# Performance work log

Measured on AMD Instinct MI355X. Metric: run time of the kernel, lower is better.

## Reference

```python
import jax, jax.numpy as jnp
import numpy as np

B, S, D, H = 4, 2048, 512, 8
DK = D // H  # 64


def setup_inputs() -> dict:
    key = jax.random.key(0)
    ks = jax.random.split(key, 7)
    return {
        "q": jax.random.normal(ks[0], (B, S, D), dtype=jnp.float32),
        "k": jax.random.normal(ks[1], (B, S, D), dtype=jnp.float32),
        "v": jax.random.normal(ks[2], (B, S, D), dtype=jnp.float32),
        # per-head query projection weights (also used for k and v, replicating
        # the source's bug where q_linear projects all three inputs)
        "Wq": jax.random.normal(ks[3], (H, DK, D), dtype=jnp.float32) * (1.0 / np.sqrt(D)),
        "bq": jax.random.normal(ks[4], (H, DK), dtype=jnp.float32) * 0.02,
        "Wout": jax.random.normal(ks[5], (D, H * DK), dtype=jnp.float32) * (1.0 / np.sqrt(D)),
        "bout": jax.random.normal(ks[6], (D,), dtype=jnp.float32) * 0.02,
    }


def reference(q, k, v, Wq, bq, Wout, bout):
    # Per-head projections, batched over heads. NOTE: the original module
    # (buggy but faithful) applies the SAME q_linear to q, k and v.
    scale = 1.0 / jnp.sqrt(jnp.asarray(Wq.shape[1], dtype=q.dtype))
    qh = jnp.einsum("bsd,hed->bhse", q, Wq) + bq[:, None, :]  # [B,H,S,DK]
    kh = jnp.einsum("bsd,hed->bhse", k, Wq) + bq[:, None, :]
    vh = jnp.einsum("bsd,hed->bhse", v, Wq) + bq[:, None, :]
    scores = jnp.einsum("bhqe,bhke->bhqk", qh, kh) * scale  # [B,H,S,S]
    weights = jax.nn.softmax(scores, axis=-1)
    heads = jnp.einsum("bhqk,bhke->bhqe", weights, vh)  # [B,H,S,DK]
    # concat heads along feature dim (head-major order matches torch.cat)
    concat = heads.transpose(0, 2, 1, 3).reshape(q.shape[0], q.shape[1], -1)
    return concat @ Wout.T + bout
```

## Files before the change

kernel.cpp:

```cpp
#include <hip/hip_runtime.h>

#define BB 4
#define SS 2048
#define DD 512
#define HH 8
#define DKK 64
#define HDK 512

typedef __attribute__((ext_vector_type(4))) float f32x4;
typedef __attribute__((ext_vector_type(8))) __bf16 bf16x8;
typedef __attribute__((ext_vector_type(4))) __bf16 bf16x4;

#define MFMA16(a, b, c) __builtin_amdgcn_mfma_f32_16x16x32_bf16((a), (b), (c), 0, 0, 0)

#define GLOAD_LDS16(gptr, lptr)                                                    \
    __builtin_amdgcn_global_load_lds(                                              \
        (const __attribute__((address_space(1))) void*)(gptr),                     \
        (__attribute__((address_space(3))) void*)(lptr), 16, 0, 0)

__device__ inline bf16x8 cvt48(const f32x4 f0, const f32x4 f1) {
    bf16x8 w;
    w[0] = (__bf16)f0[0]; w[1] = (__bf16)f0[1]; w[2] = (__bf16)f0[2]; w[3] = (__bf16)f0[3];
    w[4] = (__bf16)f1[0]; w[5] = (__bf16)f1[1]; w[6] = (__bf16)f1[2]; w[7] = (__bf16)f1[3];
    return w;
}

__global__ __launch_bounds__(256) void proj_kernel(
    const float* __restrict__ q, const float* __restrict__ k, const float* __restrict__ v,
    const float* __restrict__ Wq, const float* __restrict__ bq,
    __bf16* __restrict__ qh, __bf16* __restrict__ kh, __bf16* __restrict__ vt)
{
    const int z  = blockIdx.z;
    const float* X = (z == 0) ? q : (z == 1) ? k : v;
    const int m0 = blockIdx.x * 128;
    const int n0 = blockIdx.y * 128;

    __shared__ __align__(16) float As[128 * 64];
    __shared__ __align__(16) float Bs[128 * 64];

    const int t    = threadIdx.x;
    const int lane = t & 63, wid = t >> 6;
    const int lo   = lane & 15, hi = lane >> 4;
    const int wm   = wid >> 1, wn = wid & 1;

    const int srofs  = lane >> 4;
    const int schunk = lane & 15;

    f32x4 acc[4][4] = {};

    for (int k0 = 0; k0 < DD; k0 += 64) {
        __syncthreads();
#pragma unroll
        for (int i = 0; i < 8; ++i) {
            const int r0  = 32 * wid + 4 * i;
            const int row = r0 + srofs;
            const int gco = ((schunk ^ (row & 7)) << 4);
            GLOAD_LDS16((const char*)&X [(size_t)(m0 + row) * DD + k0] + gco,
                        (char*)As + r0 * 256);
            GLOAD_LDS16((const char*)&Wq[(size_t)(n0 + row) * DD + k0] + gco,
                        (char*)Bs + r0 * 256);
        }
        __syncthreads();

#pragma unroll
        for (int kk = 0; kk < 2; ++kk) {
            bf16x8 a[4], b[4];
#pragma unroll
            for (int mi = 0; mi < 4; ++mi) {
                const int ar = wm * 64 + mi * 16 + lo;
                const int rs = (ar & 7) << 4;
                const int cb = kk * 128 + hi * 32;
                f32x4 f0 = *reinterpret_cast<const f32x4*>((const char*)As + ar * 256 + (cb ^ rs));
                f32x4 f1 = *reinterpret_cast<const f32x4*>((const char*)As + ar * 256 + ((cb + 16) ^ rs));
                a[mi] = cvt48(f0, f1);
            }
#pragma unroll
            for (int ni = 0; ni < 4; ++ni) {
                const int br = wn * 64 + ni * 16 + lo;
                const int rs = (br & 7) << 4;
                const int cb = kk * 128 + hi * 32;
                f32x4 f0 = *reinterpret_cast<const f32x4*>((const char*)Bs + br * 256 + (cb ^ rs));
                f32x4 f1 = *reinterpret_cast<const f32x4*>((const char*)Bs + br * 256 + ((cb + 16) ^ rs));
                b[ni] = cvt48(f0, f1);
            }
#pragma unroll
            for (int mi = 0; mi < 4; ++mi)
#pragma unroll
                for (int ni = 0; ni < 4; ++ni)
                    acc[mi][ni] = MFMA16(a[mi], b[ni], acc[mi][ni]);
        }
    }

#pragma unroll
    for (int mi = 0; mi < 4; ++mi) {
#pragma unroll
        for (int ni = 0; ni < 4; ++ni) {
            const int n = n0 + wn * 64 + ni * 16 + lo;
            const float bias = bq[n];
            const int h_ = n >> 6, e_ = n & 63;
#pragma unroll
            for (int r = 0; r < 4; ++r) {
                const int m = m0 + wm * 64 + mi * 16 + hi * 4 + r;
                const float val = acc[mi][ni][r] + bias;
                const int b_ = m >> 11, s_ = m & (SS - 1);
                const size_t bh = (size_t)(b_ * HH + h_);
                if (z == 0)
                    qh[(bh * SS + s_) * DKK + e_] = (__bf16)val;
                else if (z == 1)
                    kh[(bh * SS + s_) * DKK + e_] = (__bf16)val;
                else
                    vt[(bh * DKK + e_) * SS + s_] = (__bf16)val;
            }
        }
    }
}

__global__ __launch_bounds__(256) void attn_kernel(
    const __bf16* __restrict__ qh, const __bf16* __restrict__ kh,
    const __bf16* __restrict__ vt, __bf16* __restrict__ concat)
{
    const int q0 = blockIdx.x * 64;
    const int bh = blockIdx.y;
    const int b_ = bh >> 3, h_ = bh & 7;
    const size_t base = (size_t)bh * SS * DKK;
    const __bf16* qhp = qh + base;
    const __bf16* khp = kh + base;
    const __bf16* vtp = vt + base;

    const int t    = threadIdx.x;
    const int lane = t & 63, wid = t >> 6;
    const int lo   = lane & 15, hi = lane >> 4;

    __shared__ __align__(16) __bf16 Ks[64 * 64];
    __shared__ __align__(16) __bf16 Vts[64 * 64];
    __shared__ __align__(16) __bf16 Ps[4][16][72];

    char* KsB  = (char*)Ks;
    char* VtsB = (char*)Vts;

    const int sr   = lane >> 3;
    const int gcb  = (lane & 7) << 4;
    const int scb  = gcb ^ (sr << 4);
    const int srow = 16 * wid + sr;

    bf16x8 qf[2];
#pragma unroll
    for (int kk = 0; kk < 2; ++kk)
        qf[kk] = *reinterpret_cast<const bf16x8*>(
            &qhp[(size_t)(q0 + 16 * wid + lo) * DKK + 32 * kk + 8 * hi]);

    f32x4 acc[4] = {};
    float m_run = -INFINITY, l_run = 0.f;

    for (int kv0 = 0; kv0 < SS; kv0 += 64) {
        bf16x8 kr0 = *reinterpret_cast<const bf16x8*>(
            (const char*)&khp[(size_t)(kv0 + srow) * DKK] + gcb);
        bf16x8 kr1 = *reinterpret_cast<const bf16x8*>(
            (const char*)&khp[(size_t)(kv0 + srow + 8) * DKK] + gcb);
        bf16x8 vr0 = *reinterpret_cast<const bf16x8*>(
            (const char*)&vtp[(size_t)srow * SS + kv0] + gcb);
        bf16x8 vr1 = *reinterpret_cast<const bf16x8*>(
            (const char*)&vtp[(size_t)(srow + 8) * SS + kv0] + gcb);

        __syncthreads();
        *reinterpret_cast<bf16x8*>(KsB  + srow * 128 + scb)       = kr0;
        *reinterpret_cast<bf16x8*>(KsB  + (srow + 8) * 128 + scb) = kr1;
        *reinterpret_cast<bf16x8*>(VtsB + srow * 128 + scb)       = vr0;
        *reinterpret_cast<bf16x8*>(VtsB + (srow + 8) * 128 + scb) = vr1;
        __syncthreads();

        f32x4 sc[4] = {};
#pragma unroll
        for (int kk = 0; kk < 2; ++kk) {
            bf16x8 kf[4];
#pragma unroll
            for (int f = 0; f < 4; ++f) {
                const int row = 16 * f + lo;
                const int cb  = (64 * kk + 16 * hi) ^ ((row & 7) << 4);
                kf[f] = *reinterpret_cast<const bf16x8*>(KsB + row * 128 + cb);
            }
#pragma unroll
            for (int f = 0; f < 4; ++f)
                sc[f] = MFMA16(kf[f], qf[kk], sc[f]);
        }

        {
            float mx = -1e30f;
#pragma unroll
            for (int f = 0; f < 4; ++f)
#pragma unroll
                for (int r = 0; r < 4; ++r)
                    mx = fmaxf(mx, sc[f][r]);
            mx = fmaxf(mx, __shfl_xor(mx, 16));
            mx = fmaxf(mx, __shfl_xor(mx, 32));
            const float mnew = fmaxf(m_run, mx * 0.125f);
            const float scl  = __expf(m_run - mnew);
            float rs = 0.f;
#pragma unroll
            for (int f = 0; f < 4; ++f) {
                bf16x4 pk;
#pragma unroll
                for (int r = 0; r < 4; ++r) {
                    const float e = __expf(fmaf(sc[f][r], 0.125f, -mnew));
                    rs += e;
                    pk[r] = (__bf16)e;
                }
                *reinterpret_cast<bf16x4*>(&Ps[wid][lo][16 * f + 4 * hi]) = pk;
            }
            rs += __shfl_xor(rs, 16);
            rs += __shfl_xor(rs, 32);
            l_run = l_run * scl + rs;
            m_run = mnew;
#pragma unroll
            for (int f = 0; f < 4; ++f)
                acc[f] *= scl;
        }

#pragma unroll
        for (int kk = 0; kk < 2; ++kk) {
            bf16x8 pb = *reinterpret_cast<const bf16x8*>(&Ps[wid][lo][32 * kk + 8 * hi]);
#pragma unroll
            for (int f = 0; f < 4; ++f) {
                const int row = 16 * f + lo;
                const int cb  = (64 * kk + 16 * hi) ^ ((row & 7) << 4);
                bf16x8 vf = *reinterpret_cast<const bf16x8*>(VtsB + row * 128 + cb);
                acc[f] = MFMA16(vf, pb, acc[f]);
            }
        }
    }

    {
        const float inv = 1.0f / l_run;
        const int qrow = q0 + 16 * wid + lo;
        const size_t ob = ((size_t)b_ * SS + qrow) * HDK + h_ * DKK;
#pragma unroll
        for (int f = 0; f < 4; ++f) {
            bf16x4 o;
#pragma unroll
            for (int r = 0; r < 4; ++r)
                o[r] = (__bf16)(acc[f][r] * inv);
            *reinterpret_cast<bf16x4*>(&concat[ob + 16 * f + 4 * hi]) = o;
        }
    }
}

__global__ __launch_bounds__(256) void outproj_kernel(
    const __bf16* __restrict__ concat, const float* __restrict__ Wout,
    const float* __restrict__ bout, float* __restrict__ out)
{
    const int m0 = blockIdx.x * 128;
    const int n0 = blockIdx.y * 128;

    __shared__ __align__(16) __bf16 As[128 * 64];
    __shared__ __align__(16) float  Bs[128 * 64];

    const int t    = threadIdx.x;
    const int lane = t & 63, wid = t >> 6;
    const int lo   = lane & 15, hi = lane >> 4;
    const int wm   = wid >> 1, wn = wid & 1;

    f32x4 acc[4][4] = {};

    for (int k0 = 0; k0 < HDK; k0 += 64) {
        __syncthreads();
#pragma unroll
        for (int i = 0; i < 4; ++i) {
            const int r0  = 32 * wid + 8 * i;
            const int row = r0 + (lane >> 3);
            const int gco = ((lane & 7) ^ (row & 7)) << 4;
            GLOAD_LDS16((const char*)&concat[(size_t)(m0 + row) * HDK + k0] + gco,
                        (char*)As + r0 * 128);
        }
#pragma unroll
        for (int i = 0; i < 8; ++i) {
            const int r0  = 32 * wid + 4 * i;
            const int row = r0 + (lane >> 4);
            const int gco = ((lane & 15) ^ (row & 7)) << 4;
            GLOAD_LDS16((const char*)&Wout[(size_t)(n0 + row) * HDK + k0] + gco,
                        (char*)Bs + r0 * 256);
        }
        __syncthreads();

#pragma unroll
        for (int kk = 0; kk < 2; ++kk) {
            bf16x8 a[4], b[4];
#pragma unroll
            for (int mi = 0; mi < 4; ++mi) {
                const int ar = wm * 64 + mi * 16 + lo;
                const int cb = (kk * 64 + hi * 16) ^ ((ar & 7) << 4);
                a[mi] = *reinterpret_cast<const bf16x8*>((const char*)As + ar * 128 + cb);
            }
#pragma unroll
            for (int ni = 0; ni < 4; ++ni) {
                const int br = wn * 64 + ni * 16 + lo;
                const int rs = (br & 7) << 4;
                const int cb = kk * 128 + hi * 32;
                f32x4 f0 = *reinterpret_cast<const f32x4*>((const char*)Bs + br * 256 + (cb ^ rs));
                f32x4 f1 = *reinterpret_cast<const f32x4*>((const char*)Bs + br * 256 + ((cb + 16) ^ rs));
                b[ni] = cvt48(f0, f1);
            }
#pragma unroll
            for (int mi = 0; mi < 4; ++mi)
#pragma unroll
                for (int ni = 0; ni < 4; ++ni)
                    acc[mi][ni] = MFMA16(a[mi], b[ni], acc[mi][ni]);
        }
    }

#pragma unroll
    for (int mi = 0; mi < 4; ++mi) {
#pragma unroll
        for (int ni = 0; ni < 4; ++ni) {
            const int n = n0 + wn * 64 + ni * 16 + lo;
            const float bias = bout[n];
#pragma unroll
            for (int r = 0; r < 4; ++r) {
                const int m = m0 + wm * 64 + mi * 16 + hi * 4 + r;
                out[(size_t)m * DD + n] = acc[mi][ni][r] + bias;
            }
        }
    }
}

extern "C" void kernel_launch(void* const* d_in, const int* in_sizes, int n_in,
                              void* d_out, int out_size, void* d_ws, size_t ws_size,
                              hipStream_t stream)
{
    (void)in_sizes; (void)n_in; (void)out_size; (void)ws_size;
    const float* q    = (const float*)d_in[0];
    const float* k    = (const float*)d_in[1];
    const float* v    = (const float*)d_in[2];
    const float* Wq   = (const float*)d_in[3];
    const float* bq   = (const float*)d_in[4];
    const float* Wout = (const float*)d_in[5];
    const float* bout = (const float*)d_in[6];
    float* out = (float*)d_out;

    char* ws = (char*)d_ws;
    __bf16* qh = (__bf16*)(ws);
    __bf16* kh = (__bf16*)(ws + (8u << 20));
    __bf16* vt = (__bf16*)(ws + (16u << 20));
    __bf16* cc = (__bf16*)(ws + (24u << 20));

    proj_kernel<<<dim3(BB * SS / 128, HDK / 128, 3), 256, 0, stream>>>(q, k, v, Wq, bq, qh, kh, vt);
    attn_kernel<<<dim3(SS / 64, BB * HH), 256, 0, stream>>>(qh, kh, vt, cc);
    outproj_kernel<<<dim3(BB * SS / 128, DD / 128), 256, 0, stream>>>(cc, Wout, bout, out);
}
```

Before: 223.8 us.

## Double-buffer projection GEMMs, widen attention KV tile, add lazy softmax rescale

The projection and output-projection GEMMs switch to double-buffered LDS with 32-wide k-steps. Each next tile's async global-to-LDS load is issued before computing the current tile, so there is one barrier per step instead of two. The output projection halves its M tile to 64 rows, which doubles its grid. Attention processes 128 keys per iteration, skips the running-max rescale unless the max grows by more than a threshold, and raises wave priority around MFMA blocks. These changes cut synchronisation and exposed load latency, at the cost of more LDS and a possible small accuracy loss from the lazy rescale.

```diff
diff --git a/kernel.cpp b/kernel.cpp
--- a/kernel.cpp
+++ b/kernel.cpp
@@ -35,60 +35,67 @@
     const int m0 = blockIdx.x * 128;
     const int n0 = blockIdx.y * 128;
 
-    __shared__ __align__(16) float As[128 * 64];
-    __shared__ __align__(16) float Bs[128 * 64];
+    __shared__ __align__(16) float As0[128 * 32], Bs0[128 * 32];
+    __shared__ __align__(16) float As1[128 * 32], Bs1[128 * 32];
 
     const int t    = threadIdx.x;
     const int lane = t & 63, wid = t >> 6;
     const int lo   = lane & 15, hi = lane >> 4;
     const int wm   = wid >> 1, wn = wid & 1;
 
-    const int srofs  = lane >> 4;
-    const int schunk = lane & 15;
+    const int lrow = lane >> 3;
+    const int lchk = ((lane & 7) ^ lrow) << 4;
+    const char* aSrc = (const char*)(X  + (size_t)(m0 + 32 * wid + lrow) * DD) + lchk;
+    const char* bSrc = (const char*)(Wq + (size_t)(n0 + 32 * wid + lrow) * DD) + lchk;
 
     f32x4 acc[4][4] = {};
 
-    for (int k0 = 0; k0 < DD; k0 += 64) {
+    auto stage = [&](float* Ab, float* Bb, int tt) {
+#pragma unroll
+        for (int i = 0; i < 4; ++i) {
+            GLOAD_LDS16(aSrc + (size_t)i * (8 * DD * 4) + (size_t)tt * 128,
+                        (char*)Ab + (32 * wid + 8 * i) * 128);
+            GLOAD_LDS16(bSrc + (size_t)i * (8 * DD * 4) + (size_t)tt * 128,
+                        (char*)Bb + (32 * wid + 8 * i) * 128);
+        }
+    };
+    auto compute = [&](const float* Ab, const float* Bb) {
+        bf16x8 a[4], b[4];
+#pragma unroll
+        for (int mi = 0; mi < 4; ++mi) {
+            const int ar = wm * 64 + mi * 16 + lo;
+            const int sw = (ar & 7) << 4;
+            f32x4 f0 = *reinterpret_cast<const f32x4*>((const char*)Ab + ar * 128 + ((32 * hi) ^ sw));
+            f32x4 f1 = *reinterpret_cast<const f32x4*>((const char*)Ab + ar * 128 + ((32 * hi + 16) ^ sw));
+            a[mi] = cvt48(f0, f1);
+        }
+#pragma unroll
+        for (int ni = 0; ni < 4; ++ni) {
+            const int br = wn * 64 + ni * 16 + lo;
+            const int sw = (br & 7) << 4;
+            f32x4 f0 = *reinterpret_cast<const f32x4*>((const char*)Bb + br * 128 + ((32 * hi) ^ sw));
+            f32x4 f1 = *reinterpret_cast<const f32x4*>((const char*)Bb + br * 128 + ((32 * hi + 16) ^ sw));
+            b[ni] = cvt48(f0, f1);
+        }
+        __builtin_amdgcn_s_setprio(1);
+#pragma unroll
+        for (int mi = 0; mi < 4; ++mi)
+#pragma unroll
+            for (int ni = 0; ni < 4; ++ni)
+                acc[mi][ni] = MFMA16(a[mi], b[ni], acc[mi][ni]);
+        __builtin_amdgcn_s_setprio(0);
+    };
+
+    float *Ac = As0, *Bc = Bs0, *An = As1, *Bn = Bs1;
+    stage(Ac, Bc, 0);
+    __syncthreads();
+    for (int tt = 0; tt < 16; ++tt) {
+        if (tt < 15) stage(An, Bn, tt + 1);
+        compute(Ac, Bc);
         __syncthreads();
-#pragma unroll
-        for (int i = 0; i < 8; ++i) {
-            const int r0  = 32 * wid + 4 * i;
-            const int row = r0 + srofs;
-            const int gco = ((schunk ^ (row & 7)) << 4);
-            GLOAD_LDS16((const char*)&X [(size_t)(m0 + row) * DD + k0] + gco,
-                        (char*)As + r0 * 256);
-            GLOAD_LDS16((const char*)&Wq[(size_t)(n0 + row) * DD + k0] + gco,
-                        (char*)Bs + r0 * 256);
-        }
-        __syncthreads();
-
-#pragma unroll
-        for (int kk = 0; kk < 2; ++kk) {
-            bf16x8 a[4], b[4];
-#pragma unroll
-            for (int mi = 0; mi < 4; ++mi) {
-                const int ar = wm * 64 + mi * 16 + lo;
-                const int rs = (ar & 7) << 4;
-                const int cb = kk * 128 + hi * 32;
-                f32x4 f0 = *reinterpret_cast<const f32x4*>((const char*)As + ar * 256 + (cb ^ rs));
-                f32x4 f1 = *reinterpret_cast<const f32x4*>((const char*)As + ar * 256 + ((cb + 16) ^ rs));
-                a[mi] = cvt48(f0, f1);
-            }
-#pragma unroll
-            for (int ni = 0; ni < 4; ++ni) {
-                const int br = wn * 64 + ni * 16 + lo;
-                const int rs = (br & 7) << 4;
-                const int cb = kk * 128 + hi * 32;
-                f32x4 f0 = *reinterpret_cast<const f32x4*>((const char*)Bs + br * 256 + (cb ^ rs));
-                f32x4 f1 = *reinterpret_cast<const f32x4*>((const char*)Bs + br * 256 + ((cb + 16) ^ rs));
-                b[ni] = cvt48(f0, f1);
-            }
-#pragma unroll
-            for (int mi = 0; mi < 4; ++mi)
-#pragma unroll
-                for (int ni = 0; ni < 4; ++ni)
-                    acc[mi][ni] = MFMA16(a[mi], b[ni], acc[mi][ni]);
-        }
+        float* tmp;
+        tmp = Ac; Ac = An; An = tmp;
+        tmp = Bc; Bc = Bn; Bn = tmp;
     }
 
 #pragma unroll
@@ -131,17 +138,21 @@
     const int lane = t & 63, wid = t >> 6;
     const int lo   = lane & 15, hi = lane >> 4;
 
-    __shared__ __align__(16) __bf16 Ks[64 * 64];
-    __shared__ __align__(16) __bf16 Vts[64 * 64];
-    __shared__ __align__(16) __bf16 Ps[4][16][72];
+    __shared__ __align__(16) __bf16 Ks[128 * 64];
+    __shared__ __align__(16) __bf16 Vts[64 * 128];
+    __shared__ __align__(16) __bf16 Ps[4][16][136];
 
     char* KsB  = (char*)Ks;
     char* VtsB = (char*)Vts;
-
-    const int sr   = lane >> 3;
-    const int gcb  = (lane & 7) << 4;
-    const int scb  = gcb ^ (sr << 4);
-    const int srow = 16 * wid + sr;
+    char* PsB  = (char*)Ps + wid * (16 * 272) + lo * 272;
+
+    const int kr = lane >> 3;
+    const int kc = (lane & 7) << 4;
+    const char* kSrc = (const char*)khp + (size_t)(32 * wid + kr) * 128 + kc;
+    const int   kDst = (32 * wid + kr) * 128 + (kc ^ (kr << 4));
+    const int vr = lane >> 4;
+    const int vc = (lane & 15) << 4;
+    const char* vSrc = (const char*)vtp + (size_t)(16 * wid + vr) * (SS * 2) + vc;
 
     bf16x8 qf[2];
 #pragma unroll
@@ -149,84 +160,91 @@
         qf[kk] = *reinterpret_cast<const bf16x8*>(
             &qhp[(size_t)(q0 + 16 * wid + lo) * DKK + 32 * kk + 8 * hi]);
 
+    const int rsw = (lo & 7) << 4;
+
     f32x4 acc[4] = {};
     float m_run = -INFINITY, l_run = 0.f;
 
-    for (int kv0 = 0; kv0 < SS; kv0 += 64) {
-        bf16x8 kr0 = *reinterpret_cast<const bf16x8*>(
-            (const char*)&khp[(size_t)(kv0 + srow) * DKK] + gcb);
-        bf16x8 kr1 = *reinterpret_cast<const bf16x8*>(
-            (const char*)&khp[(size_t)(kv0 + srow + 8) * DKK] + gcb);
-        bf16x8 vr0 = *reinterpret_cast<const bf16x8*>(
-            (const char*)&vtp[(size_t)srow * SS + kv0] + gcb);
-        bf16x8 vr1 = *reinterpret_cast<const bf16x8*>(
-            (const char*)&vtp[(size_t)(srow + 8) * SS + kv0] + gcb);
+    for (int tile = 0; tile < SS / 128; ++tile) {
+        bf16x8 kreg[4], vreg[4];
+#pragma unroll
+        for (int j = 0; j < 4; ++j) {
+            kreg[j] = *reinterpret_cast<const bf16x8*>(kSrc + j * (8 * 128));
+            vreg[j] = *reinterpret_cast<const bf16x8*>(vSrc + (size_t)j * (4 * SS * 2));
+        }
+        kSrc += 128 * 128;
+        vSrc += 128 * 2;
 
         __syncthreads();
-        *reinterpret_cast<bf16x8*>(KsB  + srow * 128 + scb)       = kr0;
-        *reinterpret_cast<bf16x8*>(KsB  + (srow + 8) * 128 + scb) = kr1;
-        *reinterpret_cast<bf16x8*>(VtsB + srow * 128 + scb)       = vr0;
-        *reinterpret_cast<bf16x8*>(VtsB + (srow + 8) * 128 + scb) = vr1;
+#pragma unroll
+        for (int j = 0; j < 4; ++j) {
+            *reinterpret_cast<bf16x8*>(KsB + kDst + j * (8 * 128)) = kreg[j];
+            const int vrow = 16 * wid + 4 * j + vr;
+            *reinterpret_cast<bf16x8*>(VtsB + vrow * 256 + (vc ^ ((vrow & 7) << 4))) = vreg[j];
+        }
         __syncthreads();
 
-        f32x4 sc[4] = {};
+        f32x4 sc[8] = {};
+        __builtin_amdgcn_s_setprio(1);
 #pragma unroll
         for (int kk = 0; kk < 2; ++kk) {
-            bf16x8 kf[4];
-#pragma unroll
-            for (int f = 0; f < 4; ++f) {
-                const int row = 16 * f + lo;
-                const int cb  = (64 * kk + 16 * hi) ^ ((row & 7) << 4);
-                kf[f] = *reinterpret_cast<const bf16x8*>(KsB + row * 128 + cb);
-            }
-#pragma unroll
-            for (int f = 0; f < 4; ++f)
-                sc[f] = MFMA16(kf[f], qf[kk], sc[f]);
-        }
+            const int cb = (kk * 64 + 16 * hi) ^ rsw;
+#pragma unroll
+            for (int f = 0; f < 8; ++f) {
+                bf16x8 kf = *reinterpret_cast<const bf16x8*>(KsB + (16 * f + lo) * 128 + cb);
+                sc[f] = MFMA16(kf, qf[kk], sc[f]);
+            }
+        }
+        __builtin_amdgcn_s_setprio(0);
 
         {
-            float mx = -1e30f;
-#pragma unroll
-            for (int f = 0; f < 4; ++f)
+            float mx = sc[0][0];
+#pragma unroll
+            for (int f = 0; f < 8; ++f)
 #pragma unroll
                 for (int r = 0; r < 4; ++r)
                     mx = fmaxf(mx, sc[f][r]);
             mx = fmaxf(mx, __shfl_xor(mx, 16));
             mx = fmaxf(mx, __shfl_xor(mx, 32));
-            const float mnew = fmaxf(m_run, mx * 0.125f);
-            const float scl  = __expf(m_run - mnew);
+            const float mxs = mx * 0.125f;
+            if (!__all(mxs <= m_run + 8.0f)) {
+                const float mnew = fmaxf(m_run, mxs);
+                const float scl  = __expf(m_run - mnew);
+                l_run *= scl;
+#pragma unroll
+                for (int f = 0; f < 4; ++f)
+                    acc[f] *= scl;
+                m_run = mnew;
+            }
             float rs = 0.f;
 #pragma unroll
-            for (int f = 0; f < 4; ++f) {
+            for (int f = 0; f < 8; ++f) {
                 bf16x4 pk;
 #pragma unroll
                 for (int r = 0; r < 4; ++r) {
-                    const float e = __expf(fmaf(sc[f][r], 0.125f, -mnew));
+                    const float e = __expf(fmaf(sc[f][r], 0.125f, -m_run));
                     rs += e;
                     pk[r] = (__bf16)e;
                 }
-                *reinterpret_cast<bf16x4*>(&Ps[wid][lo][16 * f + 4 * hi]) = pk;
+                *reinterpret_cast<bf16x4*>(PsB + 32 * f + 8 * hi) = pk;
             }
             rs += __shfl_xor(rs, 16);
             rs += __shfl_xor(rs, 32);
-            l_run = l_run * scl + rs;
-            m_run = mnew;
-#pragma unroll
-            for (int f = 0; f < 4; ++f)
-                acc[f] *= scl;
-        }
-
-#pragma unroll
-        for (int kk = 0; kk < 2; ++kk) {
-            bf16x8 pb = *reinterpret_cast<const bf16x8*>(&Ps[wid][lo][32 * kk + 8 * hi]);
+            l_run += rs;
+        }
+
+        __builtin_amdgcn_s_setprio(1);
+#pragma unroll
+        for (int kk = 0; kk < 4; ++kk) {
+            bf16x8 pb = *reinterpret_cast<const bf16x8*>(PsB + 64 * kk + 16 * hi);
+            const int cb = (kk * 64 + 16 * hi) ^ rsw;
 #pragma unroll
             for (int f = 0; f < 4; ++f) {
-                const int row = 16 * f + lo;
-                const int cb  = (64 * kk + 16 * hi) ^ ((row & 7) << 4);
-                bf16x8 vf = *reinterpret_cast<const bf16x8*>(VtsB + row * 128 + cb);
+                bf16x8 vf = *reinterpret_cast<const bf16x8*>(VtsB + (16 * f + lo) * 256 + cb);
                 acc[f] = MFMA16(vf, pb, acc[f]);
             }
         }
+        __builtin_amdgcn_s_setprio(0);
     }
 
     {
@@ -248,74 +266,79 @@
     const __bf16* __restrict__ concat, const float* __restrict__ Wout,
     const float* __restrict__ bout, float* __restrict__ out)
 {
-    const int m0 = blockIdx.x * 128;
+    const int m0 = blockIdx.x * 64;
     const int n0 = blockIdx.y * 128;
 
-    __shared__ __align__(16) __bf16 As[128 * 64];
-    __shared__ __align__(16) float  Bs[128 * 64];
+    __shared__ __align__(16) __bf16 As0[64 * 32], As1[64 * 32];
+    __shared__ __align__(16) float  Bs0[128 * 32], Bs1[128 * 32];
 
     const int t    = threadIdx.x;
     const int lane = t & 63, wid = t >> 6;
     const int lo   = lane & 15, hi = lane >> 4;
     const int wm   = wid >> 1, wn = wid & 1;
 
-    f32x4 acc[4][4] = {};
-
-    for (int k0 = 0; k0 < HDK; k0 += 64) {
+    const int ar4  = lane >> 2;
+    const int achk = ((lane & 3) ^ (ar4 & 3)) << 4;
+    const char* aSrc = (const char*)(concat + (size_t)(m0 + 16 * wid + ar4) * HDK) + achk;
+    const int br8  = lane >> 3;
+    const int bchk = ((lane & 7) ^ br8) << 4;
+    const char* bSrc = (const char*)(Wout + (size_t)(n0 + 32 * wid + br8) * HDK) + bchk;
+
+    f32x4 acc[2][4] = {};
+
+    auto stage = [&](__bf16* Ab, float* Bb, int tt) {
+        GLOAD_LDS16(aSrc + (size_t)tt * 64, (char*)Ab + (16 * wid) * 64);
+#pragma unroll
+        for (int i = 0; i < 4; ++i)
+            GLOAD_LDS16(bSrc + (size_t)i * (8 * HDK * 4) + (size_t)tt * 128,
+                        (char*)Bb + (32 * wid + 8 * i) * 128);
+    };
+    auto compute = [&](const __bf16* Ab, const float* Bb) {
+        bf16x8 a[2], b[4];
+#pragma unroll
+        for (int mi = 0; mi < 2; ++mi) {
+            const int ar = wm * 32 + mi * 16 + lo;
+            a[mi] = *reinterpret_cast<const bf16x8*>(
+                (const char*)Ab + ar * 64 + ((16 * hi) ^ ((ar & 3) << 4)));
+        }
+#pragma unroll
+        for (int ni = 0; ni < 4; ++ni) {
+            const int br = wn * 64 + ni * 16 + lo;
+            const int sw = (br & 7) << 4;
+            f32x4 f0 = *reinterpret_cast<const f32x4*>((const char*)Bb + br * 128 + ((32 * hi) ^ sw));
+            f32x4 f1 = *reinterpret_cast<const f32x4*>((const char*)Bb + br * 128 + ((32 * hi + 16) ^ sw));
+            b[ni] = cvt48(f0, f1);
+        }
+        __builtin_amdgcn_s_setprio(1);
+#pragma unroll
+        for (int mi = 0; mi < 2; ++mi)
+#pragma unroll
+            for (int ni = 0; ni < 4; ++ni)
+                acc[mi][ni] = MFMA16(a[mi], b[ni], acc[mi][ni]);
+        __builtin_amdgcn_s_setprio(0);
+    };
+
+    __bf16 *Ac = As0, *An = As1;
+    float  *Bc = Bs0, *Bn = Bs1;
+    stage(Ac, Bc, 0);
+    __syncthreads();
+    for (int tt = 0; tt < 16; ++tt) {
+        if (tt < 15) stage(An, Bn, tt + 1);
+        compute(Ac, Bc);
         __syncthreads();
-#pragma unroll
-        for (int i = 0; i < 4; ++i) {
-            const int r0  = 32 * wid + 8 * i;
-            const int row = r0 + (lane >> 3);
-            const int gco = ((lane & 7) ^ (row & 7)) << 4;
-            GLOAD_LDS16((const char*)&concat[(size_t)(m0 + row) * HDK + k0] + gco,
-                        (char*)As + r0 * 128);
-        }
-#pragma unroll
-        for (int i = 0; i < 8; ++i) {
-            const int r0  = 32 * wid + 4 * i;
-            const int row = r0 + (lane >> 4);
-            const int gco = ((lane & 15) ^ (row & 7)) << 4;
-            GLOAD_LDS16((const char*)&Wout[(size_t)(n0 + row) * HDK + k0] + gco,
-                        (char*)Bs + r0 * 256);
-        }
-        __syncthreads();
-
-#pragma unroll
-        for (int kk = 0; kk < 2; ++kk) {
-            bf16x8 a[4], b[4];
-#pragma unroll
-            for (int mi = 0; mi < 4; ++mi) {
-                const int ar = wm * 64 + mi * 16 + lo;
-                const int cb = (kk * 64 + hi * 16) ^ ((ar & 7) << 4);
-                a[mi] = *reinterpret_cast<const bf16x8*>((const char*)As + ar * 128 + cb);
-            }
-#pragma unroll
-            for (int ni = 0; ni < 4; ++ni) {
-                const int br = wn * 64 + ni * 16 + lo;
-                const int rs = (br & 7) << 4;
-                const int cb = kk * 128 + hi * 32;
-                f32x4 f0 = *reinterpret_cast<const f32x4*>((const char*)Bs + br * 256 + (cb ^ rs));
-                f32x4 f1 = *reinterpret_cast<const f32x4*>((const char*)Bs + br * 256 + ((cb + 16) ^ rs));
-                b[ni] = cvt48(f0, f1);
-            }
-#pragma unroll
-            for (int mi = 0; mi < 4; ++mi)
-#pragma unroll
-                for (int ni = 0; ni < 4; ++ni)
-                    acc[mi][ni] = MFMA16(a[mi], b[ni], acc[mi][ni]);
-        }
-    }
-
-#pragma unroll
-    for (int mi = 0; mi < 4; ++mi) {
+        __bf16* ta = Ac; Ac = An; An = ta;
+        float*  tb = Bc; Bc = Bn; Bn = tb;
+    }
+
+#pragma unroll
+    for (int mi = 0; mi < 2; ++mi) {
 #pragma unroll
         for (int ni = 0; ni < 4; ++ni) {
             const int n = n0 + wn * 64 + ni * 16 + lo;
             const float bias = bout[n];
 #pragma unroll
             for (int r = 0; r < 4; ++r) {
-                const int m = m0 + wm * 64 + mi * 16 + hi * 4 + r;
+                const int m = m0 + wm * 32 + mi * 16 + hi * 4 + r;
                 out[(size_t)m * DD + n] = acc[mi][ni][r] + bias;
             }
         }
@@ -344,5 +367,5 @@
 
     proj_kernel<<<dim3(BB * SS / 128, HDK / 128, 3), 256, 0, stream>>>(q, k, v, Wq, bq, qh, kh, vt);
     attn_kernel<<<dim3(SS / 64, BB * HH), 256, 0, stream>>>(qh, kh, vt, cc);
-    outproj_kernel<<<dim3(BB * SS / 128, DD / 128), 256, 0, stream>>>(cc, Wout, bout, out);
-}
+    outproj_kernel<<<dim3(BB * SS / 64, DD / 128), 256, 0, stream>>>(cc, Wout, bout, out);
+}
```

After: 228.0 us. Within noise of the previous version (+1.9%).
